# Performance work log

Hardware: AMD Instinct MI355X
Metric: run time of the kernel (lower is better)

The kernel has to match this reference:

```python
import jax, jax.numpy as jnp
import numpy as np

D = 128      # flattened state dim (n_dim)
T = 128      # time grid length
N = 32       # quadrature nodes per integral
H = 256      # func MLP hidden
HK = 64      # kernel MLP hidden
ITERS = 3    # IDESolver max_iterations


def setup_inputs() -> dict:
    key = jax.random.key(0)
    ks = jax.random.split(key, 6)
    z0 = jax.random.normal(ks[0], (1, D), jnp.float32)
    t = jnp.linspace(0.0, 1.0, T, dtype=jnp.float32)
    W1 = jax.random.normal(ks[1], (D, H), jnp.float32) / np.float32(np.sqrt(D))
    b1 = jnp.zeros((H,), jnp.float32)
    W2 = jax.random.normal(ks[2], (H, D), jnp.float32) / np.float32(np.sqrt(H))
    b2 = jnp.zeros((D,), jnp.float32)
    Wk1 = jax.random.normal(ks[3], (2, HK), jnp.float32) / np.float32(np.sqrt(2))
    bk1 = jnp.zeros((HK,), jnp.float32)
    # small kernel init keeps the Picard iteration stable
    Wk2 = jax.random.normal(ks[4], (HK, D * D), jnp.float32) * np.float32(0.01 / np.sqrt(HK))
    bk2 = jnp.zeros((D * D,), jnp.float32)
    return dict(z0=z0, t=t, W1=W1, b1=b1, W2=W2, b2=b2,
                Wk1=Wk1, bk1=bk1, Wk2=Wk2, bk2=bk2)


def _spline_coeffs(x, y):
    # natural cubic spline second derivatives M: tridiagonal system, natural BC
    n = x.shape[0]
    h = x[1:] - x[:-1]                       # [T-1]
    A = jnp.zeros((n, n), y.dtype).at[0, 0].set(1.0).at[n - 1, n - 1].set(1.0)
    idx = jnp.arange(1, n - 1)
    A = A.at[idx, idx - 1].set(h[:-1])
    A = A.at[idx, idx].set(2.0 * (h[:-1] + h[1:]))
    A = A.at[idx, idx + 1].set(h[1:])
    slope = (y[1:] - y[:-1]) / h[:, None]
    rhs = jnp.zeros_like(y).at[1:-1].set(6.0 * (slope[1:] - slope[:-1]))
    return jnp.linalg.solve(A, rhs)          # [T, D]


def _spline_eval(x, y, M, q):
    # evaluate spline at flat query points q [Q] -> [Q, D]
    qc = jnp.clip(q, x[0], x[-1])
    i = jnp.clip(jnp.searchsorted(x, qc, side='right') - 1, 0, x.shape[0] - 2)
    h = x[i + 1] - x[i]
    a = (x[i + 1] - qc) / h
    b = (qc - x[i]) / h
    return (a[:, None] * y[i] + b[:, None] * y[i + 1]
            + ((a ** 3 - a)[:, None] * M[i] + (b ** 3 - b)[:, None] * M[i + 1])
            * (h ** 2 / 6.0)[:, None])


def _F(y, W1, b1, W2, b2):
    return jnp.tanh(y @ W1 + b1) @ W2 + b2


def _K(ts, Wk1, bk1, Wk2, bk2):
    # ts [..., 2] -> kernel matrices [..., D, D]
    hden = jnp.tanh(ts @ Wk1 + bk1)
    return (hden @ Wk2 + bk2).reshape(ts.shape[:-1] + (D, D))


def reference(z0, t, W1, b1, W2, b2, Wk1, bk1, Wk2, bk2):
    y0 = z0.reshape(-1)                          # solver state: flattened z0 [D]
    u = jnp.linspace(0.0, 1.0, N, dtype=t.dtype) # unit quad nodes
    wq = jnp.ones((N,), t.dtype).at[0].set(0.5).at[-1].set(0.5)  # trapezoid
    mids = 0.5 * (t[:-1] + t[1:])
    xs = jnp.concatenate([t, mids])              # eval points [P = 2T-1]
    hstep = t[1:] - t[:-1]
    yg = jnp.broadcast_to(y0, (T, D))            # Picard initial guess y^(0)=y0
    for _ in range(ITERS):
        M = _spline_coeffs(t, yg)
        s = xs[:, None] * u[None, :]                              # [P, N], lb=0, ub=x
        ys = _spline_eval(t, yg, M, s.reshape(-1)).reshape(-1, N, D)
        fy = _F(ys, W1, b1, W2, b2)                               # [P, N, D]
        ts = jnp.stack([jnp.broadcast_to(xs[:, None], s.shape), s], -1)
        k = _K(ts, Wk1, bk1, Wk2, bk2)                            # [P, N, D, D]
        integ = jnp.einsum('pnij,pnj->pni', k, fy)
        g = jnp.einsum('pni,n->pi', integ, wq) * (xs / (N - 1))[:, None]  # [P, D]
        g_t, g_m = g[:T], g[T:]
        # Simpson (== RK4 for y-independent RHS) + cumulative integration
        inc = (hstep[:, None] / 6.0) * (g_t[:-1] + 4.0 * g_m + g_t[1:])
        yg = y0[None, :] + jnp.concatenate(
            [jnp.zeros((1, D), yg.dtype), jnp.cumsum(inc, axis=0)])
    return yg[:, None, :]                        # [T, 1, D] like solver.y.unsqueeze(1)
```

## Files before the change

kernel.cpp:

```cpp
#include <hip/hip_runtime.h>
#include <hip/hip_fp16.h>

#define D_  128
#define T_  128
#define P_  255
#define SROW 8320
#define GSZ  32640

#define OFF_YGT   0
#define OFF_COEF  8192
#define OFF_AINV  8704
#define OFF_E     41472
#define OFF_HDW   563712
#define OFF_W1T   828912
#define OFF_W2T   845296
#define OFF_WTT   861680
#define OFF_S     1394160
#define OFF_G2    2459120
#define OFF_CTR   2491760

typedef _Float16 f16;
typedef _Float16 f16x4 __attribute__((ext_vector_type(4)));
typedef float f32x4 __attribute__((ext_vector_type(4)));

__device__ __forceinline__ float tanh_fast(float x) {
  float e = __expf(2.0f * x);
  return 1.0f - 2.0f / (e + 1.0f);
}

__device__ __forceinline__ f16x4 ldfrag(const f16* buf, int row, int kunits,
                                        int kk, int quad) {
  int u = row * kunits + ((kk * 4 + quad) ^ (row & 7));
  return *(const f16x4*)(buf + 4 * u);
}

__global__ __launch_bounds__(256) void k_setup(
    const float* __restrict__ z0, const float* __restrict__ tgrid,
    const float* __restrict__ W1, const float* __restrict__ W2,
    const float* __restrict__ Wk2, const float* __restrict__ bk2,
    __half* __restrict__ ygT, float* __restrict__ coef,
    float* __restrict__ Ainv, __half* __restrict__ W1T,
    __half* __restrict__ W2T, __half* __restrict__ WTT,
    unsigned* __restrict__ ctr) {
  __shared__ __align__(16) unsigned char smem[66560];
  int bid = blockIdx.x, tid = threadIdx.x;
  for (int idx = bid * 256 + tid; idx < 65 * 16384; idx += 256 * 256) {
    int c = idx >> 14, rem = idx & 16383;
    int i = rem >> 7, j = rem & 127;
    float v = (c < 64) ? Wk2[idx] : bk2[rem];
    WTT[i * 8320 + c * 128 + j] = __float2half(v);
  }
  if (bid == 0) {
    for (int idx = tid; idx < 16384; idx += 256) {
      int grow = idx >> 7, d = idx & 127;
      ygT[d * 128 + grow] = __float2half(z0[d]);
    }
  } else if (bid == 1) {
    for (int idx = tid; idx < 32768; idx += 256) {
      int c = idx >> 7, d = idx & 127;
      W1T[idx] = __float2half(W1[d * 256 + c]);
    }
  } else if (bid == 2) {
    for (int idx = tid; idx < 32768; idx += 256) {
      int j = idx >> 8, c2 = idx & 255;
      W2T[idx] = __float2half(W2[c2 * 128 + j]);
    }
  } else if (bid == 3) {
    if (tid == 0) *ctr = 0u;
  } else if (bid == 255) {
    float* dpL = (float*)smem;
    float* tl  = (float*)(smem + 65024);
    float* cpL = tl + 128;
    float* imL = cpL + 128;
    if (tid < 128) tl[tid] = tgrid[tid];
    __syncthreads();
    if (tid == 0) {
      cpL[0] = 0.0f;
      float cprev = 0.0f;
      for (int i = 1; i <= 126; ++i) {
        float hm = tl[i] - tl[i - 1], hi = tl[i + 1] - tl[i];
        float m = 2.0f * (hm + hi) - hm * cprev;
        float im = 1.0f / m;
        imL[i] = im;
        cprev = hi * im;
        cpL[i] = cprev;
      }
    }
    if (tid < 127) coef[256 + tid] = 1.0f / (tl[tid + 1] - tl[tid]);
    __syncthreads();
    if (tid < 128) {
      int d = tid;
      float dprev = (d == 0) ? 1.0f : 0.0f;
      dpL[d] = dprev;
      for (int i = 1; i <= 126; ++i) {
        float rhs = (i == d) ? 1.0f : 0.0f;
        float hm = tl[i] - tl[i - 1];
        dprev = (rhs - hm * dprev) * imL[i];
        dpL[i * 128 + d] = dprev;
      }
      float x = (d == 127) ? 1.0f : 0.0f;
      Ainv[127 * 128 + d] = x;
      for (int i = 126; i >= 0; --i) {
        x = dpL[i * 128 + d] - cpL[i] * x;
        Ainv[i * 128 + d] = x;
      }
    }
  }
}

__global__ __launch_bounds__(256) void k_EH(const float* __restrict__ t,
                                            const float* __restrict__ Wk1,
                                            const float* __restrict__ bk1,
                                            const float* __restrict__ coef,
                                            const float* __restrict__ Ainv,
                                            __half* __restrict__ E,
                                            __half* __restrict__ HDW) {
  __shared__ float tl[128], ihL[128];
  __shared__ float sn[32], an[32], bn[32], cA[32], cB[32];
  __shared__ int idn[32];
  int p = blockIdx.x, tid = threadIdx.x;
  if (tid < 128) tl[tid] = t[tid];
  if (tid < 127) ihL[tid] = coef[256 + tid];
  __syncthreads();
  float xp = (p < T_) ? tl[p] : 0.5f * (tl[p - T_] + tl[p - T_ + 1]);
  if (tid < 32) {
    int n = tid;
    float u = (float)n * (1.0f / 31.0f);
    float q = xp * u;
    float qc = fminf(fmaxf(q, tl[0]), tl[127]);
    int i = (int)floorf(qc * 127.0f);
    i = max(0, min(126, i));
    while (i > 0 && qc < tl[i]) --i;
    while (i < 126 && qc >= tl[i + 1]) ++i;
    float h = tl[i + 1] - tl[i];
    float aa = (tl[i + 1] - qc) / h, bb = (qc - tl[i]) / h;
    sn[n] = q; idn[n] = i; an[n] = aa; bn[n] = bb;
    float h26 = h * h * (1.0f / 6.0f);
    cA[n] = (aa * aa * aa - aa) * h26;
    cB[n] = (bb * bb * bb - bb) * h26;
  }
  __syncthreads();
  #pragma unroll
  for (int pass = 0; pass < 16; ++pass) {
    int n = pass * 2 + (tid >> 7);
    int b = tid & 127;
    int i = idn[n];
    float Gi = 0.0f, Gi1 = 0.0f;
    if (b >= 2) {
      float w = 6.0f * ihL[b - 1];
      Gi  += Ainv[i * 128 + b - 1] * w;
      Gi1 += Ainv[(i + 1) * 128 + b - 1] * w;
    }
    if (b >= 1 && b <= 126) {
      float w = -6.0f * (ihL[b - 1] + ihL[b]);
      Gi  += Ainv[i * 128 + b] * w;
      Gi1 += Ainv[(i + 1) * 128 + b] * w;
    }
    if (b <= 125) {
      float w = 6.0f * ihL[b];
      Gi  += Ainv[i * 128 + b + 1] * w;
      Gi1 += Ainv[(i + 1) * 128 + b + 1] * w;
    }
    float v = cA[n] * Gi + cB[n] * Gi1;
    if (b == i) v += an[n];
    if (b == i + 1) v += bn[n];
    E[(p * 32 + n) * 128 + b] = __float2half(v);
  }
  #pragma unroll
  for (int k = 0; k < 9; ++k) {
    int idx = k * 256 + tid;
    if (idx < 2080) {
      int c = idx >> 5, n = idx & 31;
      float wq = (n == 0 || n == 31) ? 0.5f : 1.0f;
      float v = (c < 64)
          ? wq * tanh_fast(fmaf(xp, Wk1[c], fmaf(sn[n], Wk1[64 + c], bk1[c])))
          : wq;
      HDW[p * 2080 + idx] = __float2half(v);
    }
  }
}

__global__ __launch_bounds__(512) void k_fused(
    const __half* __restrict__ ygT, const __half* __restrict__ E,
    const __half* __restrict__ HDW,
    const __half* __restrict__ W1T, const __half* __restrict__ W2T,
    const float* __restrict__ b1, const float* __restrict__ b2,
    __half* __restrict__ Sh, float* __restrict__ g) {
  __shared__ __align__(16) unsigned char smem[65536];
  f16* RW = (f16*)smem;
  f16* RA = (f16*)(smem + 32768);
  f16* RB = (f16*)(smem + 40960);
  f16* RC = (f16*)(smem + 49152);
  int p = blockIdx.x, tid = threadIdx.x;
  int wv = tid >> 6, l = tid & 63, quad = l >> 4, r = l & 15;

  if (tid < 128) g[p * 128 + tid] = 0.0f;
  if (p == 0) {
    unsigned* zrow = (unsigned*)(Sh + 255 * SROW);
    for (int z = tid; z < SROW / 2; z += 512) zrow[z] = 0u;
  }

  uint2 pf[8];
  uint2 pfh[2];
  {
    const uint2* s1 = (const uint2*)W1T;
    #pragma unroll
    for (int k = 0; k < 8; ++k) pf[k] = s1[k * 512 + tid];
  }
  {
    const uint2* src = (const uint2*)ygT;
    uint2* dst = (uint2*)RW;
    #pragma unroll
    for (int k = 0; k < 8; ++k) {
      int idx = k * 512 + tid;
      int row = idx >> 5, k4 = idx & 31;
      dst[row * 32 + (k4 ^ (row & 7))] = src[idx];
    }
    const uint2* se = (const uint2*)(E + p * 4096);
    uint2* da = (uint2*)RA;
    #pragma unroll
    for (int k = 0; k < 2; ++k) {
      int idx = k * 512 + tid;
      int row = idx >> 5, k4 = idx & 31;
      da[row * 32 + (k4 ^ (row & 7))] = se[idx];
    }
  }
  __syncthreads();
  for (int tt = wv; tt < 16; tt += 8) {
    int mt = tt >> 3, nt = tt & 7;
    f32x4 acc = {0.f, 0.f, 0.f, 0.f};
    #pragma unroll
    for (int kk = 0; kk < 8; ++kk) {
      f16x4 av = ldfrag(RA, mt * 16 + r, 32, kk, quad);
      f16x4 bv = ldfrag(RW, nt * 16 + r, 32, kk, quad);
      acc = __builtin_amdgcn_mfma_f32_16x16x16f16(av, bv, acc, 0, 0, 0);
    }
    int col = nt * 16 + r;
    #pragma unroll
    for (int i = 0; i < 4; ++i) {
      int row = mt * 16 + quad * 4 + i;
      RB[row * 128 + (col ^ ((row & 7) << 2))] = (f16)acc[i];
    }
  }
  __syncthreads();
  {
    uint2* dst = (uint2*)RW;
    #pragma unroll
    for (int k = 0; k < 8; ++k) {
      int idx = k * 512 + tid;
      int row = idx >> 5, k4 = idx & 31;
      dst[row * 32 + (k4 ^ (row & 7))] = pf[k];
    }
    const uint2* s1 = (const uint2*)(W1T + 16384);
    #pragma unroll
    for (int k = 0; k < 8; ++k) pf[k] = s1[k * 512 + tid];
  }
  __syncthreads();
  for (int tt = wv; tt < 16; tt += 8) {
    int mt = tt >> 3, nt = tt & 7;
    f32x4 acc = {0.f, 0.f, 0.f, 0.f};
    #pragma unroll
    for (int kk = 0; kk < 8; ++kk) {
      f16x4 av = ldfrag(RB, mt * 16 + r, 32, kk, quad);
      f16x4 bv = ldfrag(RW, nt * 16 + r, 32, kk, quad);
      acc = __builtin_amdgcn_mfma_f32_16x16x16f16(av, bv, acc, 0, 0, 0);
    }
    int colg = nt * 16 + r;
    float bias = b1[colg];
    #pragma unroll
    for (int i = 0; i < 4; ++i) {
      int row = mt * 16 + quad * 4 + i;
      RC[row * 256 + (colg ^ ((row & 7) << 2))] = (f16)tanh_fast(acc[i] + bias);
    }
  }
  __syncthreads();
  {
    uint2* dst = (uint2*)RW;
    #pragma unroll
    for (int k = 0; k < 8; ++k) {
      int idx = k * 512 + tid;
      int row = idx >> 5, k4 = idx & 31;
      dst[row * 32 + (k4 ^ (row & 7))] = pf[k];
    }
    const uint2* sh_ = (const uint2*)(HDW + p * 2080);
    #pragma unroll
    for (int k = 0; k < 2; ++k) {
      int idx = k * 512 + tid;
      if (idx < 640) pfh[k] = (idx < 520) ? sh_[idx] : make_uint2(0u, 0u);
    }
    const uint2* s2 = (const uint2*)W2T;
    #pragma unroll
    for (int k = 0; k < 8; ++k) pf[k] = s2[k * 512 + tid];
  }
  __syncthreads();
  for (int tt = wv; tt < 16; tt += 8) {
    int mt = tt >> 3, nt = tt & 7;
    f32x4 acc = {0.f, 0.f, 0.f, 0.f};
    #pragma unroll
    for (int kk = 0; kk < 8; ++kk) {
      f16x4 av = ldfrag(RB, mt * 16 + r, 32, kk, quad);
      f16x4 bv = ldfrag(RW, nt * 16 + r, 32, kk, quad);
      acc = __builtin_amdgcn_mfma_f32_16x16x16f16(av, bv, acc, 0, 0, 0);
    }
    int colg = 128 + nt * 16 + r;
    float bias = b1[colg];
    #pragma unroll
    for (int i = 0; i < 4; ++i) {
      int row = mt * 16 + quad * 4 + i;
      RC[row * 256 + (colg ^ ((row & 7) << 2))] = (f16)tanh_fast(acc[i] + bias);
    }
  }
  __syncthreads();
  {
    uint2* db = (uint2*)RB;
    #pragma unroll
    for (int k = 0; k < 2; ++k) {
      int idx = k * 512 + tid;
      if (idx < 640) {
        int row = idx >> 3, k4 = idx & 7;
        db[row * 8 + (k4 ^ (row & 7))] = pfh[k];
      }
    }
    uint2* dst = (uint2*)RW;
    #pragma unroll
    for (int k = 0; k < 8; ++k) {
      int idx = k * 512 + tid;
      int row = idx >> 6, k4 = idx & 63;
      dst[row * 64 + (k4 ^ (row & 7))] = pf[k];
    }
    const uint2* s2 = (const uint2*)(W2T + 16384);
    #pragma unroll
    for (int k = 0; k < 8; ++k) pf[k] = s2[k * 512 + tid];
  }
  __syncthreads();
  for (int tt = wv; tt < 8; tt += 8) {
    int mt = tt >> 2, nt = tt & 3;
    f32x4 acc = {0.f, 0.f, 0.f, 0.f};
    #pragma unroll
    for (int kk = 0; kk < 16; ++kk) {
      f16x4 av = ldfrag(RC, mt * 16 + r, 64, kk, quad);
      f16x4 bv = ldfrag(RW, nt * 16 + r, 64, kk, quad);
      acc = __builtin_amdgcn_mfma_f32_16x16x16f16(av, bv, acc, 0, 0, 0);
    }
    int jg = nt * 16 + r;
    float bias = b2[jg];
    #pragma unroll
    for (int i = 0; i < 4; ++i) {
      int n = mt * 16 + quad * 4 + i;
      RA[jg * 32 + (n ^ ((jg & 7) << 2))] = (f16)(acc[i] + bias);
    }
  }
  __syncthreads();
  {
    uint2* dst = (uint2*)RW;
    #pragma unroll
    for (int k = 0; k < 8; ++k) {
      int idx = k * 512 + tid;
      int row = idx >> 6, k4 = idx & 63;
      dst[row * 64 + (k4 ^ (row & 7))] = pf[k];
    }
  }
  __syncthreads();
  for (int tt = wv; tt < 8; tt += 8) {
    int mt = tt >> 2, nt = tt & 3;
    f32x4 acc = {0.f, 0.f, 0.f, 0.f};
    #pragma unroll
    for (int kk = 0; kk < 16; ++kk) {
      f16x4 av = ldfrag(RC, mt * 16 + r, 64, kk, quad);
      f16x4 bv = ldfrag(RW, nt * 16 + r, 64, kk, quad);
      acc = __builtin_amdgcn_mfma_f32_16x16x16f16(av, bv, acc, 0, 0, 0);
    }
    int jg = 64 + nt * 16 + r;
    float bias = b2[jg];
    #pragma unroll
    for (int i = 0; i < 4; ++i) {
      int n = mt * 16 + quad * 4 + i;
      RA[jg * 32 + (n ^ ((jg & 7) << 2))] = (f16)(acc[i] + bias);
    }
  }
  __syncthreads();
  for (int tt = wv; tt < 40; tt += 8) {
    int mt = tt >> 3, nt = tt & 7;
    f32x4 acc = {0.f, 0.f, 0.f, 0.f};
    #pragma unroll
    for (int kk = 0; kk < 2; ++kk) {
      f16x4 av = ldfrag(RB, mt * 16 + r, 8, kk, quad);
      f16x4 bv = ldfrag(RA, nt * 16 + r, 8, kk, quad);
      acc = __builtin_amdgcn_mfma_f32_16x16x16f16(av, bv, acc, 0, 0, 0);
    }
    #pragma unroll
    for (int i = 0; i < 4; ++i) {
      int c = mt * 16 + quad * 4 + i;
      if (c < 65) Sh[p * SROW + c * 128 + nt * 16 + r] = __float2half(acc[i]);
    }
  }
}

__global__ __launch_bounds__(256) void k_gemmM(
    const __half* __restrict__ Sh, const __half* __restrict__ WTT,
    float* __restrict__ g, const float* __restrict__ t,
    const float* __restrict__ z0, __half* __restrict__ ygT,
    float* __restrict__ out, unsigned* __restrict__ ctr, int wout) {
  __shared__ __align__(16) unsigned char smem[65280];
  __shared__ unsigned lastFlag;
  uint2* Asw  = (uint2*)smem;
  uint2* Bsw0 = (uint2*)(smem + 20480);
  uint2* Bsw1 = (uint2*)(smem + 36864);
  int mt = blockIdx.x;
  int kc = blockIdx.y;
  int tid = threadIdx.x;
  int wv = tid >> 6, l = tid & 63, quad = l >> 4, r = l & 15;
  int p0 = mt * 16;
  int k0 = kc * 640;
  int rowT = tid >> 4, u4lo = tid & 15;
  {
    const uint2* srcA = (const uint2*)(Sh + (p0 + rowT) * SROW + k0) + u4lo;
    #pragma unroll
    for (int pass = 0; pass < 10; ++pass) {
      int u4 = pass * 16 + u4lo;
      Asw[rowT * 160 + (u4 ^ (rowT & 7))] = srcA[pass * 16];
    }
  }
  #pragma unroll
  for (int pass = 0; pass < 8; ++pass) {
    int n = pass * 16 + rowT;
    Bsw0[n * 16 + (u4lo ^ (n & 7))] = *((const uint2*)(WTT + n * SROW + k0) + u4lo);
  }
  __syncthreads();
  f32x4 acc0 = {0.f, 0.f, 0.f, 0.f}, acc1 = {0.f, 0.f, 0.f, 0.f};
  int n0 = wv * 32;
  const f16* Af = (const f16*)Asw;
  for (int kb = 0; kb < 10; ++kb) {
    const f16* Bf = (const f16*)((kb & 1) ? Bsw1 : Bsw0);
    uint2* nxtB = (kb & 1) ? Bsw0 : Bsw1;
    uint2 pf[8];
    if (kb < 9) {
      #pragma unroll
      for (int pass = 0; pass < 8; ++pass) {
        int n = pass * 16 + rowT;
        pf[pass] = *((const uint2*)(WTT + n * SROW + k0 + (kb + 1) * 64) + u4lo);
      }
    }
    #pragma unroll
    for (int kk = 0; kk < 4; ++kk) {
      int kg4 = kb * 16 + kk * 4 + quad;
      f16x4 av = *(const f16x4*)(Af + 4 * (r * 160 + (kg4 ^ (r & 7))));
      int nr0 = n0 + r, nr1 = n0 + 16 + r;
      f16x4 b0 = *(const f16x4*)(Bf + 4 * (nr0 * 16 + ((kk * 4 + quad) ^ (nr0 & 7))));
      f16x4 b1 = *(const f16x4*)(Bf + 4 * (nr1 * 16 + ((kk * 4 + quad) ^ (nr1 & 7))));
      acc0 = __builtin_amdgcn_mfma_f32_16x16x16f16(av, b0, acc0, 0, 0, 0);
      acc1 = __builtin_amdgcn_mfma_f32_16x16x16f16(av, b1, acc1, 0, 0, 0);
    }
    __syncthreads();
    if (kb < 9) {
      #pragma unroll
      for (int pass = 0; pass < 8; ++pass) {
        int n = pass * 16 + rowT;
        nxtB[n * 16 + (u4lo ^ (n & 7))] = pf[pass];
      }
      __syncthreads();
    }
  }
  #pragma unroll
  for (int i = 0; i < 4; ++i) {
    int p = p0 + quad * 4 + i;
    if (p < 255) {
      atomicAdd(&g[p * 128 + n0 + r], acc0[i]);
      atomicAdd(&g[p * 128 + n0 + 16 + r], acc1[i]);
    }
  }
  __threadfence();
  if (tid == 0) {
    unsigned old = atomicAdd(ctr, 1u);
    lastFlag = (old == 207u) ? 1u : 0u;
    if (lastFlag) *ctr = 0u;
  }
  __syncthreads();
  if (!lastFlag) return;
  __threadfence();
  float* incL = (float*)smem;
  for (int idx = tid; idx < 127 * 128; idx += 256) {
    int k = idx >> 7, d = idx & 127;
    float tk = t[k], tk1 = t[k + 1];
    float h = tk1 - tk;
    float sct  = tk * (1.0f / 31.0f);
    float scm  = 0.5f * (tk + tk1) * (1.0f / 31.0f);
    float sct1 = tk1 * (1.0f / 31.0f);
    incL[idx] = h * (1.0f / 6.0f) *
        (g[k * 128 + d] * sct + 4.0f * g[(T_ + k) * 128 + d] * scm +
         g[(k + 1) * 128 + d] * sct1);
  }
  __syncthreads();
  if (tid < 128) {
    int d = tid;
    float acc = z0[d];
    ygT[d * 128] = __float2half(acc);
    if (wout) out[d] = acc;
    #pragma unroll 4
    for (int k = 0; k < 127; ++k) {
      acc += incL[k * 128 + d];
      ygT[d * 128 + k + 1] = __float2half(acc);
      if (wout) out[(k + 1) * 128 + d] = acc;
    }
  }
}

extern "C" void kernel_launch(void* const* d_in, const int* in_sizes, int n_in,
                              void* d_out, int out_size, void* d_ws, size_t ws_size,
                              hipStream_t stream) {
  const float* z0  = (const float*)d_in[0];
  const float* t   = (const float*)d_in[1];
  const float* W1  = (const float*)d_in[2];
  const float* b1  = (const float*)d_in[3];
  const float* W2  = (const float*)d_in[4];
  const float* b2  = (const float*)d_in[5];
  const float* Wk1 = (const float*)d_in[6];
  const float* bk1 = (const float*)d_in[7];
  const float* Wk2 = (const float*)d_in[8];
  const float* bk2 = (const float*)d_in[9];
  float* out = (float*)d_out;
  float* ws  = (float*)d_ws;

  __half*   ygT  = (__half*)(ws + OFF_YGT);
  float*    coef = ws + OFF_COEF;
  float*    Ainv = ws + OFF_AINV;
  __half*   E    = (__half*)(ws + OFF_E);
  __half*   HDW  = (__half*)(ws + OFF_HDW);
  __half*   W1T  = (__half*)(ws + OFF_W1T);
  __half*   W2T  = (__half*)(ws + OFF_W2T);
  __half*   WTT  = (__half*)(ws + OFF_WTT);
  __half*   Sh   = (__half*)(ws + OFF_S);
  float*    g    = ws + OFF_G2;
  unsigned* ctr  = (unsigned*)(ws + OFF_CTR);

  k_setup<<<dim3(256), dim3(256), 0, stream>>>(z0, t, W1, W2, Wk2, bk2,
                                               ygT, coef, Ainv, W1T, W2T, WTT,
                                               ctr);
  k_EH<<<dim3(255), dim3(256), 0, stream>>>(t, Wk1, bk1, coef, Ainv, E, HDW);
  for (int it = 0; it < 3; ++it) {
    k_fused<<<dim3(255), dim3(512), 0, stream>>>(ygT, E, HDW, W1T, W2T,
                                                 b1, b2, Sh, g);
    k_gemmM<<<dim3(16, 13), dim3(256), 0, stream>>>(Sh, WTT, g, t, z0, ygT, out,
                                                    ctr, (it == 2) ? 1 : 0);
  }
}
```

Measured before the change: 185.9 us.

## Merge EH and Picard iteration kernels into one persistent kernel with grid barriers

Replaces the k_EH launch and the six per-iteration k_fused/k_gemmM launches with a single persistent 255-block kernel that uses atomic-counter grid barriers between phases. The intent is to remove kernel launch gaps and tail effects between the many short phases. The GEMM phase is remapped onto 512-thread blocks with 16 columns per wave, and the final cumulative-sum step runs on block 0 after a barrier instead of a last-block counter. This relies on all 255 blocks being co-resident; otherwise the spin barriers deadlock. It also serializes phases with spin-wait barriers and leaves idle blocks during the GEMM and scan phases.

Result: slower. 368.2 us (+98.0%).

```diff
diff --git a/kernel.cpp b/kernel.cpp
--- a/kernel.cpp
+++ b/kernel.cpp
@@ -6,6 +6,7 @@
 #define P_  255
 #define SROW 8320
 #define GSZ  32640
+#define NBLK 255u
 
 #define OFF_YGT   0
 #define OFF_COEF  8192
@@ -17,7 +18,7 @@
 #define OFF_WTT   861680
 #define OFF_S     1394160
 #define OFF_G2    2459120
-#define OFF_CTR   2491760
+#define OFF_BAR   2491760
 
 typedef _Float16 f16;
 typedef _Float16 f16x4 __attribute__((ext_vector_type(4)));
@@ -32,6 +33,17 @@
                                         int kk, int quad) {
   int u = row * kunits + ((kk * 4 + quad) ^ (row & 7));
   return *(const f16x4*)(buf + 4 * u);
+}
+
+__device__ __forceinline__ void megabar(unsigned* bar, int slot) {
+  __syncthreads();
+  if (threadIdx.x == 0) {
+    __threadfence();
+    atomicAdd(&bar[slot], 1u);
+    while (atomicAdd(&bar[slot], 0u) < NBLK) __builtin_amdgcn_s_sleep(2);
+    __threadfence();
+  }
+  __syncthreads();
 }
 
 __global__ __launch_bounds__(256) void k_setup(
@@ -41,7 +53,7 @@
     __half* __restrict__ ygT, float* __restrict__ coef,
     float* __restrict__ Ainv, __half* __restrict__ W1T,
     __half* __restrict__ W2T, __half* __restrict__ WTT,
-    unsigned* __restrict__ ctr) {
+    unsigned* __restrict__ bar) {
   __shared__ __align__(16) unsigned char smem[66560];
   int bid = blockIdx.x, tid = threadIdx.x;
   for (int idx = bid * 256 + tid; idx < 65 * 16384; idx += 256 * 256) {
@@ -66,7 +78,7 @@
       W2T[idx] = __float2half(W2[c2 * 128 + j]);
     }
   } else if (bid == 3) {
-    if (tid == 0) *ctr = 0u;
+    if (tid < 16) bar[tid] = 0u;
   } else if (bid == 255) {
     float* dpL = (float*)smem;
     float* tl  = (float*)(smem + 65024);
@@ -108,400 +120,391 @@
   }
 }
 
-__global__ __launch_bounds__(256) void k_EH(const float* __restrict__ t,
-                                            const float* __restrict__ Wk1,
-                                            const float* __restrict__ bk1,
-                                            const float* __restrict__ coef,
-                                            const float* __restrict__ Ainv,
-                                            __half* __restrict__ E,
-                                            __half* __restrict__ HDW) {
+__global__ __launch_bounds__(512, 1) void k_mega(
+    const float* __restrict__ tgrid, const float* __restrict__ z0,
+    const float* __restrict__ Wk1, const float* __restrict__ bk1,
+    const float* __restrict__ b1, const float* __restrict__ b2,
+    const float* __restrict__ coef, const float* __restrict__ Ainv,
+    __half* __restrict__ E, __half* __restrict__ HDW,
+    const __half* __restrict__ W1T, const __half* __restrict__ W2T,
+    const __half* __restrict__ WTT, __half* __restrict__ ygT,
+    __half* __restrict__ Sh, float* __restrict__ g,
+    float* __restrict__ out, unsigned* __restrict__ bar) {
+  __shared__ __align__(16) unsigned char smem[65536];
   __shared__ float tl[128], ihL[128];
   __shared__ float sn[32], an[32], bn[32], cA[32], cB[32];
   __shared__ int idn[32];
-  int p = blockIdx.x, tid = threadIdx.x;
-  if (tid < 128) tl[tid] = t[tid];
-  if (tid < 127) ihL[tid] = coef[256 + tid];
-  __syncthreads();
-  float xp = (p < T_) ? tl[p] : 0.5f * (tl[p - T_] + tl[p - T_ + 1]);
-  if (tid < 32) {
-    int n = tid;
-    float u = (float)n * (1.0f / 31.0f);
-    float q = xp * u;
-    float qc = fminf(fmaxf(q, tl[0]), tl[127]);
-    int i = (int)floorf(qc * 127.0f);
-    i = max(0, min(126, i));
-    while (i > 0 && qc < tl[i]) --i;
-    while (i < 126 && qc >= tl[i + 1]) ++i;
-    float h = tl[i + 1] - tl[i];
-    float aa = (tl[i + 1] - qc) / h, bb = (qc - tl[i]) / h;
-    sn[n] = q; idn[n] = i; an[n] = aa; bn[n] = bb;
-    float h26 = h * h * (1.0f / 6.0f);
-    cA[n] = (aa * aa * aa - aa) * h26;
-    cB[n] = (bb * bb * bb - bb) * h26;
+  int bid = blockIdx.x, tid = threadIdx.x;
+  int wv = tid >> 6, l = tid & 63, quad = l >> 4, r = l & 15;
+
+  {
+    int p = bid;
+    if (tid < 128) tl[tid] = tgrid[tid];
+    if (tid < 127) ihL[tid] = coef[256 + tid];
+    __syncthreads();
+    float xp = (p < T_) ? tl[p] : 0.5f * (tl[p - T_] + tl[p - T_ + 1]);
+    if (tid < 32) {
+      int n = tid;
+      float u = (float)n * (1.0f / 31.0f);
+      float q = xp * u;
+      float qc = fminf(fmaxf(q, tl[0]), tl[127]);
+      int i = (int)floorf(qc * 127.0f);
+      i = max(0, min(126, i));
+      while (i > 0 && qc < tl[i]) --i;
+      while (i < 126 && qc >= tl[i + 1]) ++i;
+      float h = tl[i + 1] - tl[i];
+      float aa = (tl[i + 1] - qc) / h, bb = (qc - tl[i]) / h;
+      sn[n] = q; idn[n] = i; an[n] = aa; bn[n] = bb;
+      float h26 = h * h * (1.0f / 6.0f);
+      cA[n] = (aa * aa * aa - aa) * h26;
+      cB[n] = (bb * bb * bb - bb) * h26;
+    }
+    __syncthreads();
+    #pragma unroll
+    for (int pass = 0; pass < 8; ++pass) {
+      int n = pass * 4 + (tid >> 7);
+      int b = tid & 127;
+      int i = idn[n];
+      float Gi = 0.0f, Gi1 = 0.0f;
+      if (b >= 2) {
+        float w = 6.0f * ihL[b - 1];
+        Gi  += Ainv[i * 128 + b - 1] * w;
+        Gi1 += Ainv[(i + 1) * 128 + b - 1] * w;
+      }
+      if (b >= 1 && b <= 126) {
+        float w = -6.0f * (ihL[b - 1] + ihL[b]);
+        Gi  += Ainv[i * 128 + b] * w;
+        Gi1 += Ainv[(i + 1) * 128 + b] * w;
+      }
+      if (b <= 125) {
+        float w = 6.0f * ihL[b];
+        Gi  += Ainv[i * 128 + b + 1] * w;
+        Gi1 += Ainv[(i + 1) * 128 + b + 1] * w;
+      }
+      float v = cA[n] * Gi + cB[n] * Gi1;
+      if (b == i) v += an[n];
+      if (b == i + 1) v += bn[n];
+      E[(p * 32 + n) * 128 + b] = __float2half(v);
+    }
+    #pragma unroll
+    for (int k = 0; k < 5; ++k) {
+      int idx = k * 512 + tid;
+      if (idx < 2080) {
+        int c = idx >> 5, n = idx & 31;
+        float wq = (n == 0 || n == 31) ? 0.5f : 1.0f;
+        float v = (c < 64)
+            ? wq * tanh_fast(fmaf(xp, Wk1[c], fmaf(sn[n], Wk1[64 + c], bk1[c])))
+            : wq;
+        HDW[p * 2080 + idx] = __float2half(v);
+      }
+    }
   }
-  __syncthreads();
-  #pragma unroll
-  for (int pass = 0; pass < 16; ++pass) {
-    int n = pass * 2 + (tid >> 7);
-    int b = tid & 127;
-    int i = idn[n];
-    float Gi = 0.0f, Gi1 = 0.0f;
-    if (b >= 2) {
-      float w = 6.0f * ihL[b - 1];
-      Gi  += Ainv[i * 128 + b - 1] * w;
-      Gi1 += Ainv[(i + 1) * 128 + b - 1] * w;
-    }
-    if (b >= 1 && b <= 126) {
-      float w = -6.0f * (ihL[b - 1] + ihL[b]);
-      Gi  += Ainv[i * 128 + b] * w;
-      Gi1 += Ainv[(i + 1) * 128 + b] * w;
-    }
-    if (b <= 125) {
-      float w = 6.0f * ihL[b];
-      Gi  += Ainv[i * 128 + b + 1] * w;
-      Gi1 += Ainv[(i + 1) * 128 + b + 1] * w;
-    }
-    float v = cA[n] * Gi + cB[n] * Gi1;
-    if (b == i) v += an[n];
-    if (b == i + 1) v += bn[n];
-    E[(p * 32 + n) * 128 + b] = __float2half(v);
-  }
-  #pragma unroll
-  for (int k = 0; k < 9; ++k) {
-    int idx = k * 256 + tid;
-    if (idx < 2080) {
-      int c = idx >> 5, n = idx & 31;
-      float wq = (n == 0 || n == 31) ? 0.5f : 1.0f;
-      float v = (c < 64)
-          ? wq * tanh_fast(fmaf(xp, Wk1[c], fmaf(sn[n], Wk1[64 + c], bk1[c])))
-          : wq;
-      HDW[p * 2080 + idx] = __float2half(v);
-    }
-  }
-}
-
-__global__ __launch_bounds__(512) void k_fused(
-    const __half* __restrict__ ygT, const __half* __restrict__ E,
-    const __half* __restrict__ HDW,
-    const __half* __restrict__ W1T, const __half* __restrict__ W2T,
-    const float* __restrict__ b1, const float* __restrict__ b2,
-    __half* __restrict__ Sh, float* __restrict__ g) {
-  __shared__ __align__(16) unsigned char smem[65536];
-  f16* RW = (f16*)smem;
-  f16* RA = (f16*)(smem + 32768);
-  f16* RB = (f16*)(smem + 40960);
-  f16* RC = (f16*)(smem + 49152);
-  int p = blockIdx.x, tid = threadIdx.x;
-  int wv = tid >> 6, l = tid & 63, quad = l >> 4, r = l & 15;
-
-  if (tid < 128) g[p * 128 + tid] = 0.0f;
-  if (p == 0) {
-    unsigned* zrow = (unsigned*)(Sh + 255 * SROW);
-    for (int z = tid; z < SROW / 2; z += 512) zrow[z] = 0u;
-  }
-
-  uint2 pf[8];
-  uint2 pfh[2];
-  {
-    const uint2* s1 = (const uint2*)W1T;
-    #pragma unroll
-    for (int k = 0; k < 8; ++k) pf[k] = s1[k * 512 + tid];
-  }
-  {
-    const uint2* src = (const uint2*)ygT;
-    uint2* dst = (uint2*)RW;
-    #pragma unroll
-    for (int k = 0; k < 8; ++k) {
-      int idx = k * 512 + tid;
-      int row = idx >> 5, k4 = idx & 31;
-      dst[row * 32 + (k4 ^ (row & 7))] = src[idx];
-    }
-    const uint2* se = (const uint2*)(E + p * 4096);
-    uint2* da = (uint2*)RA;
-    #pragma unroll
-    for (int k = 0; k < 2; ++k) {
-      int idx = k * 512 + tid;
-      int row = idx >> 5, k4 = idx & 31;
-      da[row * 32 + (k4 ^ (row & 7))] = se[idx];
-    }
-  }
-  __syncthreads();
-  for (int tt = wv; tt < 16; tt += 8) {
-    int mt = tt >> 3, nt = tt & 7;
-    f32x4 acc = {0.f, 0.f, 0.f, 0.f};
-    #pragma unroll
-    for (int kk = 0; kk < 8; ++kk) {
-      f16x4 av = ldfrag(RA, mt * 16 + r, 32, kk, quad);
-      f16x4 bv = ldfrag(RW, nt * 16 + r, 32, kk, quad);
-      acc = __builtin_amdgcn_mfma_f32_16x16x16f16(av, bv, acc, 0, 0, 0);
-    }
-    int col = nt * 16 + r;
-    #pragma unroll
-    for (int i = 0; i < 4; ++i) {
-      int row = mt * 16 + quad * 4 + i;
-      RB[row * 128 + (col ^ ((row & 7) << 2))] = (f16)acc[i];
-    }
-  }
-  __syncthreads();
-  {
-    uint2* dst = (uint2*)RW;
-    #pragma unroll
-    for (int k = 0; k < 8; ++k) {
-      int idx = k * 512 + tid;
-      int row = idx >> 5, k4 = idx & 31;
-      dst[row * 32 + (k4 ^ (row & 7))] = pf[k];
-    }
-    const uint2* s1 = (const uint2*)(W1T + 16384);
-    #pragma unroll
-    for (int k = 0; k < 8; ++k) pf[k] = s1[k * 512 + tid];
-  }
-  __syncthreads();
-  for (int tt = wv; tt < 16; tt += 8) {
-    int mt = tt >> 3, nt = tt & 7;
-    f32x4 acc = {0.f, 0.f, 0.f, 0.f};
-    #pragma unroll
-    for (int kk = 0; kk < 8; ++kk) {
-      f16x4 av = ldfrag(RB, mt * 16 + r, 32, kk, quad);
-      f16x4 bv = ldfrag(RW, nt * 16 + r, 32, kk, quad);
-      acc = __builtin_amdgcn_mfma_f32_16x16x16f16(av, bv, acc, 0, 0, 0);
-    }
-    int colg = nt * 16 + r;
-    float bias = b1[colg];
-    #pragma unroll
-    for (int i = 0; i < 4; ++i) {
-      int row = mt * 16 + quad * 4 + i;
-      RC[row * 256 + (colg ^ ((row & 7) << 2))] = (f16)tanh_fast(acc[i] + bias);
-    }
-  }
-  __syncthreads();
-  {
-    uint2* dst = (uint2*)RW;
-    #pragma unroll
-    for (int k = 0; k < 8; ++k) {
-      int idx = k * 512 + tid;
-      int row = idx >> 5, k4 = idx & 31;
-      dst[row * 32 + (k4 ^ (row & 7))] = pf[k];
-    }
-    const uint2* sh_ = (const uint2*)(HDW + p * 2080);
-    #pragma unroll
-    for (int k = 0; k < 2; ++k) {
-      int idx = k * 512 + tid;
-      if (idx < 640) pfh[k] = (idx < 520) ? sh_[idx] : make_uint2(0u, 0u);
-    }
-    const uint2* s2 = (const uint2*)W2T;
-    #pragma unroll
-    for (int k = 0; k < 8; ++k) pf[k] = s2[k * 512 + tid];
-  }
-  __syncthreads();
-  for (int tt = wv; tt < 16; tt += 8) {
-    int mt = tt >> 3, nt = tt & 7;
-    f32x4 acc = {0.f, 0.f, 0.f, 0.f};
-    #pragma unroll
-    for (int kk = 0; kk < 8; ++kk) {
-      f16x4 av = ldfrag(RB, mt * 16 + r, 32, kk, quad);
-      f16x4 bv = ldfrag(RW, nt * 16 + r, 32, kk, quad);
-      acc = __builtin_amdgcn_mfma_f32_16x16x16f16(av, bv, acc, 0, 0, 0);
-    }
-    int colg = 128 + nt * 16 + r;
-    float bias = b1[colg];
-    #pragma unroll
-    for (int i = 0; i < 4; ++i) {
-      int row = mt * 16 + quad * 4 + i;
-      RC[row * 256 + (colg ^ ((row & 7) << 2))] = (f16)tanh_fast(acc[i] + bias);
-    }
-  }
-  __syncthreads();
-  {
-    uint2* db = (uint2*)RB;
-    #pragma unroll
-    for (int k = 0; k < 2; ++k) {
-      int idx = k * 512 + tid;
-      if (idx < 640) {
-        int row = idx >> 3, k4 = idx & 7;
-        db[row * 8 + (k4 ^ (row & 7))] = pfh[k];
-      }
-    }
-    uint2* dst = (uint2*)RW;
-    #pragma unroll
-    for (int k = 0; k < 8; ++k) {
-      int idx = k * 512 + tid;
-      int row = idx >> 6, k4 = idx & 63;
-      dst[row * 64 + (k4 ^ (row & 7))] = pf[k];
-    }
-    const uint2* s2 = (const uint2*)(W2T + 16384);
-    #pragma unroll
-    for (int k = 0; k < 8; ++k) pf[k] = s2[k * 512 + tid];
-  }
-  __syncthreads();
-  for (int tt = wv; tt < 8; tt += 8) {
-    int mt = tt >> 2, nt = tt & 3;
-    f32x4 acc = {0.f, 0.f, 0.f, 0.f};
-    #pragma unroll
-    for (int kk = 0; kk < 16; ++kk) {
-      f16x4 av = ldfrag(RC, mt * 16 + r, 64, kk, quad);
-      f16x4 bv = ldfrag(RW, nt * 16 + r, 64, kk, quad);
-      acc = __builtin_amdgcn_mfma_f32_16x16x16f16(av, bv, acc, 0, 0, 0);
-    }
-    int jg = nt * 16 + r;
-    float bias = b2[jg];
-    #pragma unroll
-    for (int i = 0; i < 4; ++i) {
-      int n = mt * 16 + quad * 4 + i;
-      RA[jg * 32 + (n ^ ((jg & 7) << 2))] = (f16)(acc[i] + bias);
-    }
-  }
-  __syncthreads();
-  {
-    uint2* dst = (uint2*)RW;
-    #pragma unroll
-    for (int k = 0; k < 8; ++k) {
-      int idx = k * 512 + tid;
-      int row = idx >> 6, k4 = idx & 63;
-      dst[row * 64 + (k4 ^ (row & 7))] = pf[k];
-    }
-  }
-  __syncthreads();
-  for (int tt = wv; tt < 8; tt += 8) {
-    int mt = tt >> 2, nt = tt & 3;
-    f32x4 acc = {0.f, 0.f, 0.f, 0.f};
-    #pragma unroll
-    for (int kk = 0; kk < 16; ++kk) {
-      f16x4 av = ldfrag(RC, mt * 16 + r, 64, kk, quad);
-      f16x4 bv = ldfrag(RW, nt * 16 + r, 64, kk, quad);
-      acc = __builtin_amdgcn_mfma_f32_16x16x16f16(av, bv, acc, 0, 0, 0);
-    }
-    int jg = 64 + nt * 16 + r;
-    float bias = b2[jg];
-    #pragma unroll
-    for (int i = 0; i < 4; ++i) {
-      int n = mt * 16 + quad * 4 + i;
-      RA[jg * 32 + (n ^ ((jg & 7) << 2))] = (f16)(acc[i] + bias);
-    }
-  }
-  __syncthreads();
-  for (int tt = wv; tt < 40; tt += 8) {
-    int mt = tt >> 3, nt = tt & 7;
-    f32x4 acc = {0.f, 0.f, 0.f, 0.f};
-    #pragma unroll
-    for (int kk = 0; kk < 2; ++kk) {
-      f16x4 av = ldfrag(RB, mt * 16 + r, 8, kk, quad);
-      f16x4 bv = ldfrag(RA, nt * 16 + r, 8, kk, quad);
-      acc = __builtin_amdgcn_mfma_f32_16x16x16f16(av, bv, acc, 0, 0, 0);
-    }
-    #pragma unroll
-    for (int i = 0; i < 4; ++i) {
-      int c = mt * 16 + quad * 4 + i;
-      if (c < 65) Sh[p * SROW + c * 128 + nt * 16 + r] = __float2half(acc[i]);
-    }
-  }
-}
-
-__global__ __launch_bounds__(256) void k_gemmM(
-    const __half* __restrict__ Sh, const __half* __restrict__ WTT,
-    float* __restrict__ g, const float* __restrict__ t,
-    const float* __restrict__ z0, __half* __restrict__ ygT,
-    float* __restrict__ out, unsigned* __restrict__ ctr, int wout) {
-  __shared__ __align__(16) unsigned char smem[65280];
-  __shared__ unsigned lastFlag;
-  uint2* Asw  = (uint2*)smem;
-  uint2* Bsw0 = (uint2*)(smem + 20480);
-  uint2* Bsw1 = (uint2*)(smem + 36864);
-  int mt = blockIdx.x;
-  int kc = blockIdx.y;
-  int tid = threadIdx.x;
-  int wv = tid >> 6, l = tid & 63, quad = l >> 4, r = l & 15;
-  int p0 = mt * 16;
-  int k0 = kc * 640;
-  int rowT = tid >> 4, u4lo = tid & 15;
-  {
-    const uint2* srcA = (const uint2*)(Sh + (p0 + rowT) * SROW + k0) + u4lo;
-    #pragma unroll
-    for (int pass = 0; pass < 10; ++pass) {
-      int u4 = pass * 16 + u4lo;
-      Asw[rowT * 160 + (u4 ^ (rowT & 7))] = srcA[pass * 16];
-    }
-  }
-  #pragma unroll
-  for (int pass = 0; pass < 8; ++pass) {
-    int n = pass * 16 + rowT;
-    Bsw0[n * 16 + (u4lo ^ (n & 7))] = *((const uint2*)(WTT + n * SROW + k0) + u4lo);
-  }
-  __syncthreads();
-  f32x4 acc0 = {0.f, 0.f, 0.f, 0.f}, acc1 = {0.f, 0.f, 0.f, 0.f};
-  int n0 = wv * 32;
-  const f16* Af = (const f16*)Asw;
-  for (int kb = 0; kb < 10; ++kb) {
-    const f16* Bf = (const f16*)((kb & 1) ? Bsw1 : Bsw0);
-    uint2* nxtB = (kb & 1) ? Bsw0 : Bsw1;
-    uint2 pf[8];
-    if (kb < 9) {
+  megabar(bar, 0);
+
+  for (int it = 0; it < 3; ++it) {
+    {
+      f16* RW = (f16*)smem;
+      f16* RA = (f16*)(smem + 32768);
+      f16* RB = (f16*)(smem + 40960);
+      f16* RC = (f16*)(smem + 49152);
+      int p = bid;
+
+      if (tid < 128) g[p * 128 + tid] = 0.0f;
+      if (p == 0) {
+        unsigned* zrow = (unsigned*)(Sh + 255 * SROW);
+        for (int z = tid; z < SROW / 2; z += 512) zrow[z] = 0u;
+      }
+
+      uint2 pf[8];
+      uint2 pfh[2];
+      {
+        const uint2* s1 = (const uint2*)W1T;
+        #pragma unroll
+        for (int k = 0; k < 8; ++k) pf[k] = s1[k * 512 + tid];
+      }
+      {
+        const uint2* src = (const uint2*)ygT;
+        uint2* dst = (uint2*)RW;
+        #pragma unroll
+        for (int k = 0; k < 8; ++k) {
+          int idx = k * 512 + tid;
+          int row = idx >> 5, k4 = idx & 31;
+          dst[row * 32 + (k4 ^ (row & 7))] = src[idx];
+        }
+        const uint2* se = (const uint2*)(E + p * 4096);
+        uint2* da = (uint2*)RA;
+        #pragma unroll
+        for (int k = 0; k < 2; ++k) {
+          int idx = k * 512 + tid;
+          int row = idx >> 5, k4 = idx & 31;
+          da[row * 32 + (k4 ^ (row & 7))] = se[idx];
+        }
+      }
+      __syncthreads();
+      for (int tt = wv; tt < 16; tt += 8) {
+        int mt = tt >> 3, nt = tt & 7;
+        f32x4 acc = {0.f, 0.f, 0.f, 0.f};
+        #pragma unroll
+        for (int kk = 0; kk < 8; ++kk) {
+          f16x4 av = ldfrag(RA, mt * 16 + r, 32, kk, quad);
+          f16x4 bv = ldfrag(RW, nt * 16 + r, 32, kk, quad);
+          acc = __builtin_amdgcn_mfma_f32_16x16x16f16(av, bv, acc, 0, 0, 0);
+        }
+        int col = nt * 16 + r;
+        #pragma unroll
+        for (int i = 0; i < 4; ++i) {
+          int row = mt * 16 + quad * 4 + i;
+          RB[row * 128 + (col ^ ((row & 7) << 2))] = (f16)acc[i];
+        }
+      }
+      __syncthreads();
+      {
+        uint2* dst = (uint2*)RW;
+        #pragma unroll
+        for (int k = 0; k < 8; ++k) {
+          int idx = k * 512 + tid;
+          int row = idx >> 5, k4 = idx & 31;
+          dst[row * 32 + (k4 ^ (row & 7))] = pf[k];
+        }
+        const uint2* s1 = (const uint2*)(W1T + 16384);
+        #pragma unroll
+        for (int k = 0; k < 8; ++k) pf[k] = s1[k * 512 + tid];
+      }
+      __syncthreads();
+      for (int tt = wv; tt < 16; tt += 8) {
+        int mt = tt >> 3, nt = tt & 7;
+        f32x4 acc = {0.f, 0.f, 0.f, 0.f};
+        #pragma unroll
+        for (int kk = 0; kk < 8; ++kk) {
+          f16x4 av = ldfrag(RB, mt * 16 + r, 32, kk, quad);
+          f16x4 bv = ldfrag(RW, nt * 16 + r, 32, kk, quad);
+          acc = __builtin_amdgcn_mfma_f32_16x16x16f16(av, bv, acc, 0, 0, 0);
+        }
+        int colg = nt * 16 + r;
+        float bias = b1[colg];
+        #pragma unroll
+        for (int i = 0; i < 4; ++i) {
+          int row = mt * 16 + quad * 4 + i;
+          RC[row * 256 + (colg ^ ((row & 7) << 2))] = (f16)tanh_fast(acc[i] + bias);
+        }
+      }
+      __syncthreads();
+      {
+        uint2* dst = (uint2*)RW;
+        #pragma unroll
+        for (int k = 0; k < 8; ++k) {
+          int idx = k * 512 + tid;
+          int row = idx >> 5, k4 = idx & 31;
+          dst[row * 32 + (k4 ^ (row & 7))] = pf[k];
+        }
+        const uint2* sh_ = (const uint2*)(HDW + p * 2080);
+        #pragma unroll
+        for (int k = 0; k < 2; ++k) {
+          int idx = k * 512 + tid;
+          if (idx < 640) pfh[k] = (idx < 520) ? sh_[idx] : make_uint2(0u, 0u);
+        }
+        const uint2* s2 = (const uint2*)W2T;
+        #pragma unroll
+        for (int k = 0; k < 8; ++k) pf[k] = s2[k * 512 + tid];
+      }
+      __syncthreads();
+      for (int tt = wv; tt < 16; tt += 8) {
+        int mt = tt >> 3, nt = tt & 7;
+        f32x4 acc = {0.f, 0.f, 0.f, 0.f};
+        #pragma unroll
+        for (int kk = 0; kk < 8; ++kk) {
+          f16x4 av = ldfrag(RB, mt * 16 + r, 32, kk, quad);
+          f16x4 bv = ldfrag(RW, nt * 16 + r, 32, kk, quad);
+          acc = __builtin_amdgcn_mfma_f32_16x16x16f16(av, bv, acc, 0, 0, 0);
+        }
+        int colg = 128 + nt * 16 + r;
+        float bias = b1[colg];
+        #pragma unroll
+        for (int i = 0; i < 4; ++i) {
+          int row = mt * 16 + quad * 4 + i;
+          RC[row * 256 + (colg ^ ((row & 7) << 2))] = (f16)tanh_fast(acc[i] + bias);
+        }
+      }
+      __syncthreads();
+      {
+        uint2* db = (uint2*)RB;
+        #pragma unroll
+        for (int k = 0; k < 2; ++k) {
+          int idx = k * 512 + tid;
+          if (idx < 640) {
+            int row = idx >> 3, k4 = idx & 7;
+            db[row * 8 + (k4 ^ (row & 7))] = pfh[k];
+          }
+        }
+        uint2* dst = (uint2*)RW;
+        #pragma unroll
+        for (int k = 0; k < 8; ++k) {
+          int idx = k * 512 + tid;
+          int row = idx >> 6, k4 = idx & 63;
+          dst[row * 64 + (k4 ^ (row & 7))] = pf[k];
+        }
+        const uint2* s2 = (const uint2*)(W2T + 16384);
+        #pragma unroll
+        for (int k = 0; k < 8; ++k) pf[k] = s2[k * 512 + tid];
+      }
+      __syncthreads();
+      for (int tt = wv; tt < 8; tt += 8) {
+        int mt = tt >> 2, nt = tt & 3;
+        f32x4 acc = {0.f, 0.f, 0.f, 0.f};
+        #pragma unroll
+        for (int kk = 0; kk < 16; ++kk) {
+          f16x4 av = ldfrag(RC, mt * 16 + r, 64, kk, quad);
+          f16x4 bv = ldfrag(RW, nt * 16 + r, 64, kk, quad);
+          acc = __builtin_amdgcn_mfma_f32_16x16x16f16(av, bv, acc, 0, 0, 0);
+        }
+        int jg = nt * 16 + r;
+        float bias = b2[jg];
+        #pragma unroll
+        for (int i = 0; i < 4; ++i) {
+          int n = mt * 16 + quad * 4 + i;
+          RA[jg * 32 + (n ^ ((jg & 7) << 2))] = (f16)(acc[i] + bias);
+        }
+      }
+      __syncthreads();
+      {
+        uint2* dst = (uint2*)RW;
+        #pragma unroll
+        for (int k = 0; k < 8; ++k) {
+          int idx = k * 512 + tid;
+          int row = idx >> 6, k4 = idx & 63;
+          dst[row * 64 + (k4 ^ (row & 7))] = pf[k];
+        }
+      }
+      __syncthreads();
+      for (int tt = wv; tt < 8; tt += 8) {
+        int mt = tt >> 2, nt = tt & 3;
+        f32x4 acc = {0.f, 0.f, 0.f, 0.f};
+        #pragma unroll
+        for (int kk = 0; kk < 16; ++kk) {
+          f16x4 av = ldfrag(RC, mt * 16 + r, 64, kk, quad);
+          f16x4 bv = ldfrag(RW, nt * 16 + r, 64, kk, quad);
+          acc = __builtin_amdgcn_mfma_f32_16x16x16f16(av, bv, acc, 0, 0, 0);
+        }
+        int jg = 64 + nt * 16 + r;
+        float bias = b2[jg];
+        #pragma unroll
+        for (int i = 0; i < 4; ++i) {
+          int n = mt * 16 + quad * 4 + i;
+          RA[jg * 32 + (n ^ ((jg & 7) << 2))] = (f16)(acc[i] + bias);
+        }
+      }
+      __syncthreads();
+      for (int tt = wv; tt < 40; tt += 8) {
+        int mt = tt >> 3, nt = tt & 7;
+        f32x4 acc = {0.f, 0.f, 0.f, 0.f};
+        #pragma unroll
+        for (int kk = 0; kk < 2; ++kk) {
+          f16x4 av = ldfrag(RB, mt * 16 + r, 8, kk, quad);
+          f16x4 bv = ldfrag(RA, nt * 16 + r, 8, kk, quad);
+          acc = __builtin_amdgcn_mfma_f32_16x16x16f16(av, bv, acc, 0, 0, 0);
+        }
+        #pragma unroll
+        for (int i = 0; i < 4; ++i) {
+          int c = mt * 16 + quad * 4 + i;
+          if (c < 65) Sh[p * SROW + c * 128 + nt * 16 + r] = __float2half(acc[i]);
+        }
+      }
+    }
+    megabar(bar, 1 + it * 3);
+
+    if (bid < 208) {
+      uint2* Asw  = (uint2*)smem;
+      uint2* Bsw0 = (uint2*)(smem + 20480);
+      uint2* Bsw1 = (uint2*)(smem + 36864);
+      int mtb = bid / 13, kc = bid % 13;
+      int p0 = mtb * 16, k0 = kc * 640;
+      if (tid < 256) {
+        int rowT = tid >> 4, u4lo = tid & 15;
+        const uint2* srcA = (const uint2*)(Sh + (p0 + rowT) * SROW + k0) + u4lo;
+        #pragma unroll
+        for (int pass = 0; pass < 10; ++pass) {
+          int u4 = pass * 16 + u4lo;
+          Asw[rowT * 160 + (u4 ^ (rowT & 7))] = srcA[pass * 16];
+        }
+      }
       #pragma unroll
-      for (int pass = 0; pass < 8; ++pass) {
-        int n = pass * 16 + rowT;
-        pf[pass] = *((const uint2*)(WTT + n * SROW + k0 + (kb + 1) * 64) + u4lo);
-      }
-    }
-    #pragma unroll
-    for (int kk = 0; kk < 4; ++kk) {
-      int kg4 = kb * 16 + kk * 4 + quad;
-      f16x4 av = *(const f16x4*)(Af + 4 * (r * 160 + (kg4 ^ (r & 7))));
-      int nr0 = n0 + r, nr1 = n0 + 16 + r;
-      f16x4 b0 = *(const f16x4*)(Bf + 4 * (nr0 * 16 + ((kk * 4 + quad) ^ (nr0 & 7))));
-      f16x4 b1 = *(const f16x4*)(Bf + 4 * (nr1 * 16 + ((kk * 4 + quad) ^ (nr1 & 7))));
-      acc0 = __builtin_amdgcn_mfma_f32_16x16x16f16(av, b0, acc0, 0, 0, 0);
-      acc1 = __builtin_amdgcn_mfma_f32_16x16x16f16(av, b1, acc1, 0, 0, 0);
-    }
-    __syncthreads();
-    if (kb < 9) {
+      for (int k = 0; k < 4; ++k) {
+        int idx = k * 512 + tid;
+        int row = idx >> 4, u4 = idx & 15;
+        Bsw0[row * 16 + (u4 ^ (row & 7))] =
+            *((const uint2*)(WTT + row * SROW + k0) + u4);
+      }
+      __syncthreads();
+      f32x4 acc0 = {0.f, 0.f, 0.f, 0.f};
+      int n0 = wv * 16;
+      const f16* Af = (const f16*)Asw;
+      for (int kb = 0; kb < 10; ++kb) {
+        const f16* Bf = (const f16*)((kb & 1) ? Bsw1 : Bsw0);
+        uint2* nxtB = (kb & 1) ? Bsw0 : Bsw1;
+        uint2 pfb[4];
+        if (kb < 9) {
+          #pragma unroll
+          for (int k = 0; k < 4; ++k) {
+            int idx = k * 512 + tid;
+            int row = idx >> 4, u4 = idx & 15;
+            pfb[k] = *((const uint2*)(WTT + row * SROW + k0 + (kb + 1) * 64) + u4);
+          }
+        }
+        #pragma unroll
+        for (int kk = 0; kk < 4; ++kk) {
+          int kg4 = kb * 16 + kk * 4 + quad;
+          f16x4 av = *(const f16x4*)(Af + 4 * (r * 160 + (kg4 ^ (r & 7))));
+          int nr0 = n0 + r;
+          f16x4 b0 = *(const f16x4*)(Bf + 4 * (nr0 * 16 + ((kk * 4 + quad) ^ (nr0 & 7))));
+          acc0 = __builtin_amdgcn_mfma_f32_16x16x16f16(av, b0, acc0, 0, 0, 0);
+        }
+        __syncthreads();
+        if (kb < 9) {
+          #pragma unroll
+          for (int k = 0; k < 4; ++k) {
+            int idx = k * 512 + tid;
+            int row = idx >> 4, u4 = idx & 15;
+            nxtB[row * 16 + (u4 ^ (row & 7))] = pfb[k];
+          }
+          __syncthreads();
+        }
+      }
       #pragma unroll
-      for (int pass = 0; pass < 8; ++pass) {
-        int n = pass * 16 + rowT;
-        nxtB[n * 16 + (u4lo ^ (n & 7))] = pf[pass];
-      }
-      __syncthreads();
-    }
-  }
-  #pragma unroll
-  for (int i = 0; i < 4; ++i) {
-    int p = p0 + quad * 4 + i;
-    if (p < 255) {
-      atomicAdd(&g[p * 128 + n0 + r], acc0[i]);
-      atomicAdd(&g[p * 128 + n0 + 16 + r], acc1[i]);
-    }
-  }
-  __threadfence();
-  if (tid == 0) {
-    unsigned old = atomicAdd(ctr, 1u);
-    lastFlag = (old == 207u) ? 1u : 0u;
-    if (lastFlag) *ctr = 0u;
-  }
-  __syncthreads();
-  if (!lastFlag) return;
-  __threadfence();
-  float* incL = (float*)smem;
-  for (int idx = tid; idx < 127 * 128; idx += 256) {
-    int k = idx >> 7, d = idx & 127;
-    float tk = t[k], tk1 = t[k + 1];
-    float h = tk1 - tk;
-    float sct  = tk * (1.0f / 31.0f);
-    float scm  = 0.5f * (tk + tk1) * (1.0f / 31.0f);
-    float sct1 = tk1 * (1.0f / 31.0f);
-    incL[idx] = h * (1.0f / 6.0f) *
-        (g[k * 128 + d] * sct + 4.0f * g[(T_ + k) * 128 + d] * scm +
-         g[(k + 1) * 128 + d] * sct1);
-  }
-  __syncthreads();
-  if (tid < 128) {
-    int d = tid;
-    float acc = z0[d];
-    ygT[d * 128] = __float2half(acc);
-    if (wout) out[d] = acc;
-    #pragma unroll 4
-    for (int k = 0; k < 127; ++k) {
-      acc += incL[k * 128 + d];
-      ygT[d * 128 + k + 1] = __float2half(acc);
-      if (wout) out[(k + 1) * 128 + d] = acc;
-    }
+      for (int i = 0; i < 4; ++i) {
+        int p = p0 + quad * 4 + i;
+        if (p < 255) atomicAdd(&g[p * 128 + n0 + r], acc0[i]);
+      }
+    }
+    megabar(bar, 2 + it * 3);
+
+    if (bid == 0) {
+      float* incL = (float*)smem;
+      for (int idx = tid; idx < 127 * 128; idx += 512) {
+        int k = idx >> 7, d = idx & 127;
+        float tk = tl[k], tk1 = tl[k + 1];
+        float h = tk1 - tk;
+        float sct  = tk * (1.0f / 31.0f);
+        float scm  = 0.5f * (tk + tk1) * (1.0f / 31.0f);
+        float sct1 = tk1 * (1.0f / 31.0f);
+        incL[idx] = h * (1.0f / 6.0f) *
+            (g[k * 128 + d] * sct + 4.0f * g[(T_ + k) * 128 + d] * scm +
+             g[(k + 1) * 128 + d] * sct1);
+      }
+      __syncthreads();
+      if (tid < 128) {
+        int d = tid;
+        float acc = z0[d];
+        ygT[d * 128] = __float2half(acc);
+        if (it == 2) out[d] = acc;
+        #pragma unroll 4
+        for (int k = 0; k < 127; ++k) {
+          acc += incL[k * 128 + d];
+          ygT[d * 128 + k + 1] = __float2half(acc);
+          if (it == 2) out[(k + 1) * 128 + d] = acc;
+        }
+      }
+    }
+    if (it < 2) megabar(bar, 3 + it * 3);
   }
 }
 
@@ -531,16 +534,12 @@
   __half*   WTT  = (__half*)(ws + OFF_WTT);
   __half*   Sh   = (__half*)(ws + OFF_S);
   float*    g    = ws + OFF_G2;
-  unsigned* ctr  = (unsigned*)(ws + OFF_CTR);
+  unsigned* bar  = (unsigned*)(ws + OFF_BAR);
 
   k_setup<<<dim3(256), dim3(256), 0, stream>>>(z0, t, W1, W2, Wk2, bk2,
                                                ygT, coef, Ainv, W1T, W2T, WTT,
-                                               ctr);
-  k_EH<<<dim3(255), dim3(256), 0, stream>>>(t, Wk1, bk1, coef, Ainv, E, HDW);
-  for (int it = 0; it < 3; ++it) {
-    k_fused<<<dim3(255), dim3(512), 0, stream>>>(ygT, E, HDW, W1T, W2T,
-                                                 b1, b2, Sh, g);
-    k_gemmM<<<dim3(16, 13), dim3(256), 0, stream>>>(Sh, WTT, g, t, z0, ygT, out,
-                                                    ctr, (it == 2) ? 1 : 0);
-  }
+                                               bar);
+  k_mega<<<dim3(255), dim3(512), 0, stream>>>(t, z0, Wk1, bk1, b1, b2,
+                                              coef, Ainv, E, HDW, W1T, W2T,
+                                              WTT, ygT, Sh, g, out, bar);
 }
```
